# Optimization experiments

Hardware: AMD Instinct MI355X
Metric: run time of the kernel (lower is better)

## Reference

```python
import jax, jax.numpy as jnp
import numpy as np

B, L1, L2, D = 64, 512, 512, 256
NEG_INF = -1e10


def _leaky(x):
    return jax.nn.leaky_relu(x, negative_slope=0.01)


def setup_inputs() -> dict:
    key = jax.random.key(0)
    ks = jax.random.split(key, 12)
    s = 1.0 / np.sqrt(D)
    s2 = 1.0 / np.sqrt(2 * D)
    return {
        "r1": jax.random.normal(ks[0], (B, L1, D), jnp.float32),
        "r2": jax.random.normal(ks[1], (B, L2, D), jnp.float32),
        "mask1": jax.random.randint(ks[2], (B, L1, 1), 0, 2, jnp.int32),
        "mask2": jax.random.randint(ks[3], (B, L2, 1), 0, 2, jnp.int32),
        # mlp params (shared for r1 and r2, as in the torch module)
        "W1": jax.random.uniform(ks[4], (D, D), jnp.float32, -s, s),
        "b1": jnp.zeros((D,), jnp.float32),
        "W2": jax.random.uniform(ks[5], (D, D), jnp.float32, -s, s),
        "b2": jnp.zeros((D,), jnp.float32),
        # compare params
        "Wc1": jax.random.uniform(ks[6], (2 * D, D), jnp.float32, -s2, s2),
        "bc1": jnp.zeros((D,), jnp.float32),
        "Wc2": jax.random.uniform(ks[7], (D, D), jnp.float32, -s, s),
        "bc2": jnp.zeros((D,), jnp.float32),
    }


def _mlp(x, W1, b1, W2, b2):
    return _leaky(_leaky(x @ W1 + b1) @ W2 + b2)


def _compare(x, Wc1, bc1, Wc2, bc2):
    return _leaky(_leaky(x @ Wc1 + bc1) @ Wc2 + bc2)


def reference(r1, r2, mask1, mask2, W1, b1, W2, b2, Wc1, bc1, Wc2, bc2):
    # dropout layers are identity in eval mode
    m1 = mask1.astype(jnp.float32)  # [B,L1,1]
    m2 = mask2.astype(jnp.float32)  # [B,L2,1]

    h1 = _mlp(r1, W1, b1, W2, b2) * m1  # [B,L1,D]
    h2 = _mlp(r2, W1, b1, W2, b2) * m2  # [B,L2,D]

    lens1 = m1.sum(axis=1)  # [B,1]
    lens2 = m2.sum(axis=1)  # [B,1]

    # pairwise validity: matmul of expanded masks is D * outer(m1, m2);
    # only the sign is used downstream.
    pair = m1[:, :, 0][:, :, None] * m2[:, :, 0][:, None, :]  # [B,L1,L2]
    valid = pair > 0
    mask_inf = jnp.where(valid, 0.0, NEG_INF)

    o = jnp.einsum('bld,bmd->blm', h1, h2) + mask_inf  # [B,L1,L2]
    vf = valid.astype(o.dtype)
    o1 = jax.nn.softmax(o, axis=2) * vf
    o2 = jax.nn.softmax(o, axis=1) * vf

    r1_c = jnp.einsum('blm,bmd->bld', o1, h2)  # [B,L1,D]
    r2_c = jnp.einsum('blm,bld->bmd', o2, h1)  # [B,L2,D]

    r1_cmp = _compare(jnp.concatenate([h1, r1_c], axis=-1), Wc1, bc1, Wc2, bc2)
    r2_cmp = _compare(jnp.concatenate([h2, r2_c], axis=-1), Wc1, bc1, Wc2, bc2)

    r1_pool = (r1_cmp * m1).sum(axis=1) / lens1  # [B,D]
    r2_pool = (r2_cmp * m2).sum(axis=1) / lens2  # [B,D]
    return (r1_pool, r2_pool)
```

## Files before the change

### kernel.cpp

```cpp
#include <hip/hip_runtime.h>
#include <math.h>


using frag  = __attribute__((ext_vector_type(8))) short;
using f32x4 = __attribute__((ext_vector_type(4))) float;

constexpr long E = 16777216L;

__device__ __forceinline__ float leaky(float x){ return x > 0.f ? x : 0.01f * x; }

__device__ __forceinline__ unsigned bf16_rne(float f){
    unsigned x = __float_as_uint(f);
    return (x + 0x7fffu + ((x >> 16) & 1u)) >> 16;
}

__device__ __forceinline__ void gload16(const void* g, void* l){
    __builtin_amdgcn_global_load_lds((const __attribute__((address_space(1))) void*)g,
                                     (__attribute__((address_space(3))) void*)l, 16, 0, 0);
}

template<int AMODE, int BMODE, int EPI, int DUALA>
__global__ __launch_bounds__(512, 4)
void gemm_k(const short* __restrict__ pa, const short* __restrict__ pa2,
            const short* __restrict__ pb, const float* __restrict__ bias,
            short* __restrict__ pc,
            const int* __restrict__ mk1, const int* __restrict__ mk2,
            int K, int K1, int lda, int ldb, int ldc,
            long sA, long sB, long sC, long PSA, long PSB, long PSC)
{
    __shared__ __align__(16) short Ah[4096], Al[4096], Bh[4096], Bl[4096];
    const int z = blockIdx.z;
    const int m0 = blockIdx.x * 128, n0 = blockIdx.y * 128;
    const int tid = threadIdx.x, lane = tid & 63, w = tid >> 6;
    const int wr = w >> 2, wc = w & 3;
    const long aoff = (long)z * sA, boff = (long)z * sB, coff = (long)z * sC;

    f32x4 acc[4][2];
#pragma unroll
    for (int i = 0; i < 4; ++i)
#pragma unroll
        for (int j = 0; j < 2; ++j) acc[i][j] = (f32x4){0.f, 0.f, 0.f, 0.f};

    for (int k0 = 0; k0 < K; k0 += 32) {
        if (AMODE == 0) {
            const short* base = pa + aoff; int kk = k0;
            if (DUALA) { if (k0 >= K1) { base = pa2 + aoff; kk = k0 - K1; } }
            const short* s = base + (long)(m0 + w * 16 + (lane & 15)) * lda + kk + (lane >> 4) * 8;
            gload16(s,       &Ah[w * 512]);
            gload16(s + PSA, &Al[w * 512]);
        } else {
            const int gr = m0 + w * 16 + (lane & 15);
            const float* f = (gr < 32768 ? (const float*)pa + (long)gr * lda
                                         : (const float*)pa2 + (long)(gr - 32768) * lda)
                             + k0 + (lane >> 4) * 8;
            float4 u = *(const float4*)f, v4 = *(const float4*)(f + 4);
            float fv[8] = {u.x, u.y, u.z, u.w, v4.x, v4.y, v4.z, v4.w};
            unsigned hu[8], lu[8];
#pragma unroll
            for (int j = 0; j < 8; ++j) {
                hu[j] = bf16_rne(fv[j]);
                lu[j] = bf16_rne(fv[j] - __uint_as_float(hu[j] << 16));
            }
            uint4 hs = {hu[0] | (hu[1] << 16), hu[2] | (hu[3] << 16), hu[4] | (hu[5] << 16), hu[6] | (hu[7] << 16)};
            uint4 ls = {lu[0] | (lu[1] << 16), lu[2] | (lu[3] << 16), lu[4] | (lu[5] << 16), lu[6] | (lu[7] << 16)};
            *(uint4*)&Ah[w * 512 + lane * 8] = hs;
            *(uint4*)&Al[w * 512 + lane * 8] = ls;
        }
        if (BMODE == 0) {
            const short* s = pb + boff + (long)(n0 + w * 16 + (lane & 15)) * ldb + k0 + (lane >> 4) * 8;
            gload16(s,       &Bh[w * 512]);
            gload16(s + PSB, &Bl[w * 512]);
        } else {
            const int kg = tid >> 7, nn = tid & 127;
            const short* s = pb + boff + (long)(k0 + kg * 8) * ldb + n0 + nn;
            unsigned hh[8], ll[8];
#pragma unroll
            for (int i = 0; i < 8; ++i) {
                hh[i] = (unsigned short)s[(long)i * ldb];
                ll[i] = (unsigned short)s[(long)i * ldb + PSB];
            }
            uint4 hw = {hh[0] | (hh[1] << 16), hh[2] | (hh[3] << 16), hh[4] | (hh[5] << 16), hh[6] | (hh[7] << 16)};
            uint4 lw = {ll[0] | (ll[1] << 16), ll[2] | (ll[3] << 16), ll[4] | (ll[5] << 16), ll[6] | (ll[7] << 16)};
            const int d = (nn >> 4) * 512 + (kg * 16 + (nn & 15)) * 8;
            *(uint4*)&Bh[d] = hw;
            *(uint4*)&Bl[d] = lw;
        }
        __syncthreads();

        frag fah[4], fal[4], fbh[2], fbl[2];
#pragma unroll
        for (int mi = 0; mi < 4; ++mi) {
            const int off = (wr * 4 + mi) * 512 + lane * 8;
            fah[mi] = *(const frag*)&Ah[off];
            fal[mi] = *(const frag*)&Al[off];
        }
#pragma unroll
        for (int ni = 0; ni < 2; ++ni) {
            const int off = (wc * 2 + ni) * 512 + lane * 8;
            fbh[ni] = *(const frag*)&Bh[off];
            fbl[ni] = *(const frag*)&Bl[off];
        }
#pragma unroll
        for (int mi = 0; mi < 4; ++mi)
#pragma unroll
            for (int ni = 0; ni < 2; ++ni) {
                acc[mi][ni] = __builtin_amdgcn_mfma_f32_16x16x32_bf16(fah[mi], fbh[ni], acc[mi][ni], 0, 0, 0);
                acc[mi][ni] = __builtin_amdgcn_mfma_f32_16x16x32_bf16(fah[mi], fbl[ni], acc[mi][ni], 0, 0, 0);
                acc[mi][ni] = __builtin_amdgcn_mfma_f32_16x16x32_bf16(fal[mi], fbh[ni], acc[mi][ni], 0, 0, 0);
            }
        __syncthreads();
    }

    float bvv[2];
    if (EPI == 2 || EPI == 3 || EPI == 4) {
#pragma unroll
        for (int ni = 0; ni < 2; ++ni) bvv[ni] = bias[n0 + wc * 32 + ni * 16 + (lane & 15)];
    }
#pragma unroll
    for (int mi = 0; mi < 4; ++mi)
#pragma unroll
        for (int ni = 0; ni < 2; ++ni) {
            const int col = n0 + wc * 32 + ni * 16 + (lane & 15);
#pragma unroll
            for (int r = 0; r < 4; ++r) {
                const int row = m0 + wr * 64 + mi * 16 + (lane >> 4) * 4 + r;
                float v = acc[mi][ni][r];
                if (EPI == 2 || EPI == 3 || EPI == 4) v = leaky(v + bvv[ni]);
                if (EPI == 3) v *= (float)(row < 32768 ? mk1[row] : mk2[row - 32768]);
                const long off = coff + (long)row * ldc + col;
                if (EPI == 0 || EPI == 4) {
                    ((float*)pc)[off] = v;
                } else {
                    unsigned hu = bf16_rne(v);
                    pc[off]       = (short)hu;
                    pc[off + PSC] = (short)bf16_rne(v - __uint_as_float(hu << 16));
                }
            }
        }
}

__global__ __launch_bounds__(256)
void wconv_k(const float* __restrict__ W, short* __restrict__ T, int Kd, long PS)
{
    const int idx = blockIdx.x * 256 + threadIdx.x;
    const int n = idx & 255, k = idx >> 8;
    const float v = W[idx];
    const unsigned hu = bf16_rne(v);
    T[(long)n * Kd + k]      = (short)hu;
    T[(long)n * Kd + k + PS] = (short)bf16_rne(v - __uint_as_float(hu << 16));
}

__global__ __launch_bounds__(256)
void softmax_row_k(const float* __restrict__ S, const int* __restrict__ m1,
                   const int* __restrict__ m2, short* __restrict__ O)
{
    const int tid = threadIdx.x;
    const int wid = tid >> 6, lane = tid & 63;
    const int gr = blockIdx.x * 4 + wid;
    const int b = gr >> 9, l = gr & 511;
    const float* srow = S + (long)gr * 512;
    short* orow = O + (long)gr * 512;
    const int rowvalid = m1[(long)b * 512 + l];
    const int* m2b = m2 + (long)b * 512;
    const int c8 = lane * 8;
    int4 ma = *(const int4*)(m2b + c8);
    int4 mb_ = *(const int4*)(m2b + c8 + 4);
    float4 va = *(const float4*)(srow + c8);
    float4 vb = *(const float4*)(srow + c8 + 4);
    float v[8] = {va.x, va.y, va.z, va.w, vb.x, vb.y, vb.z, vb.w};
    int mk[8] = {ma.x, ma.y, ma.z, ma.w, mb_.x, mb_.y, mb_.z, mb_.w};
    float mx = -3e38f;
#pragma unroll
    for (int j = 0; j < 8; ++j) if (mk[j]) mx = fmaxf(mx, v[j]);
#pragma unroll
    for (int o = 32; o; o >>= 1) mx = fmaxf(mx, __shfl_xor(mx, o));
    if (!rowvalid || mx < -1e30f) {
        uint4 zz = {0u, 0u, 0u, 0u};
        *(uint4*)&orow[c8] = zz;
        *(uint4*)&orow[c8 + E] = zz;
        return;
    }
    float e[8]; float s = 0.f;
#pragma unroll
    for (int j = 0; j < 8; ++j) { e[j] = mk[j] ? __expf(v[j] - mx) : 0.f; s += e[j]; }
#pragma unroll
    for (int o = 32; o; o >>= 1) s += __shfl_xor(s, o);
    const float inv = 1.f / s;
    unsigned short oh[8], ol[8];
#pragma unroll
    for (int j = 0; j < 8; ++j) {
        float p = e[j] * inv;
        unsigned hu = bf16_rne(p);
        oh[j] = (unsigned short)hu;
        ol[j] = (unsigned short)bf16_rne(p - __uint_as_float(hu << 16));
    }
    uint4 hs = {oh[0] | ((unsigned)oh[1] << 16), oh[2] | ((unsigned)oh[3] << 16),
                oh[4] | ((unsigned)oh[5] << 16), oh[6] | ((unsigned)oh[7] << 16)};
    uint4 ls = {ol[0] | ((unsigned)ol[1] << 16), ol[2] | ((unsigned)ol[3] << 16),
                ol[4] | ((unsigned)ol[5] << 16), ol[6] | ((unsigned)ol[7] << 16)};
    *(uint4*)&orow[c8] = hs;
    *(uint4*)&orow[c8 + E] = ls;
}

__global__ __launch_bounds__(1024)
void softmax_col_k(const float* __restrict__ S, const int* __restrict__ m1,
                   const int* __restrict__ m2, short* __restrict__ O)
{
    __shared__ float red[16][64];
    __shared__ int m1s[512];
    __shared__ unsigned tile[64][65];
    const int b = blockIdx.y;
    const int c0 = blockIdx.x * 64;
    const int tid = threadIdx.x;
    const int c = tid & 63, rq = tid >> 6;
    if (tid < 512) m1s[tid] = m1[(long)b * 512 + tid];
    const int ac = m2[(long)b * 512 + c0 + c];
    const float* Sb = S + (long)b * 262144 + c0 + c;
    __syncthreads();

    float v[32];
#pragma unroll
    for (int g = 0; g < 32; ++g) {
        const int r = g * 16 + rq;
        float val = Sb[(long)r * 512];
        v[g] = m1s[r] ? val : -3e38f;
    }
    float mx = -3e38f;
#pragma unroll
    for (int g = 0; g < 32; ++g) mx = fmaxf(mx, v[g]);
    red[rq][c] = mx;
    __syncthreads();
    float M = -3e38f;
#pragma unroll
    for (int i = 0; i < 16; ++i) M = fmaxf(M, red[i][c]);
    __syncthreads();
    float s = 0.f;
#pragma unroll
    for (int g = 0; g < 32; ++g) {
        float e = (v[g] > -1e30f) ? __expf(v[g] - M) : 0.f;
        v[g] = e;
        s += e;
    }
    red[rq][c] = s;
    __syncthreads();
    s = 0.f;
#pragma unroll
    for (int i = 0; i < 16; ++i) s += red[i][c];
    const float inv = (ac && s > 0.f) ? 1.f / s : 0.f;

    const int oc_ = tid >> 4, or_ = tid & 15;
    short* obase = O + (long)b * 262144 + (long)(c0 + oc_) * 512;
    for (int ch = 0; ch < 8; ++ch) {
        __syncthreads();
#pragma unroll
        for (int gg = 0; gg < 4; ++gg) {
            float p = v[ch * 4 + gg] * inv;
            unsigned hu = bf16_rne(p);
            unsigned lu = bf16_rne(p - __uint_as_float(hu << 16));
            tile[c][gg * 16 + rq] = (hu << 16) | lu;
        }
        __syncthreads();
        const unsigned w0 = tile[oc_][or_ * 4 + 0], w1 = tile[oc_][or_ * 4 + 1];
        const unsigned w2 = tile[oc_][or_ * 4 + 2], w3 = tile[oc_][or_ * 4 + 3];
        uint2 ph = { (w0 >> 16) | (w1 & 0xffff0000u), (w2 >> 16) | (w3 & 0xffff0000u) };
        uint2 pl = { (w0 & 0xffffu) | (w1 << 16),     (w2 & 0xffffu) | (w3 << 16) };
        *(uint2*)&obase[ch * 64 + or_ * 4]     = ph;
        *(uint2*)&obase[E + ch * 64 + or_ * 4] = pl;
    }
}

__global__ __launch_bounds__(256)
void pool_part_k(const float* __restrict__ RC, const int* __restrict__ m1,
                 const int* __restrict__ m2, float* __restrict__ part)
{
    const int rs = blockIdx.x, b = blockIdx.y, seg = blockIdx.z;
    const int* mb = (seg ? m2 : m1) + (long)b * 512;
    const float* base = RC + ((long)seg * 32768 + (long)b * 512) * 256;
    const int n = threadIdx.x;
    float acc = 0.f;
    for (int l = rs * 64; l < rs * 64 + 64; ++l)
        if (mb[l]) acc += base[(long)l * 256 + n];
    part[(((long)seg * 64 + b) * 8 + rs) * 256 + n] = acc;
}

__global__ __launch_bounds__(256)
void pool_red_k(const float* __restrict__ part, const int* __restrict__ m1,
                const int* __restrict__ m2, float* __restrict__ out)
{
    __shared__ float cr[256];
    const int g = blockIdx.x;
    const int seg = g >> 6, b = g & 63;
    const int n = threadIdx.x;
    const int* mb = (seg ? m2 : m1) + (long)b * 512;
    float s = 0.f;
#pragma unroll
    for (int i = 0; i < 8; ++i) s += part[((long)g * 8 + i) * 256 + n];
    cr[n] = (float)(mb[n] + mb[n + 256]);
    __syncthreads();
    for (int o = 128; o; o >>= 1) { if (n < o) cr[n] += cr[n + o]; __syncthreads(); }
    out[(long)g * 256 + n] = s / cr[0];
}

extern "C" void kernel_launch(void* const* d_in, const int* in_sizes, int n_in,
                              void* d_out, int out_size, void* d_ws, size_t ws_size,
                              hipStream_t stream)
{
    const float* r1  = (const float*)d_in[0];
    const float* r2  = (const float*)d_in[1];
    const int*   mk1 = (const int*)d_in[2];
    const int*   mk2 = (const int*)d_in[3];
    const float* W1  = (const float*)d_in[4];
    const float* b1  = (const float*)d_in[5];
    const float* W2  = (const float*)d_in[6];
    const float* b2  = (const float*)d_in[7];
    const float* Wc1 = (const float*)d_in[8];
    const float* bc1 = (const float*)d_in[9];
    const float* Wc2 = (const float*)d_in[10];
    const float* bc2 = (const float*)d_in[11];
    float* out = (float*)d_out;

    short* S0s = (short*)d_ws;
    short* S1s = S0s + 2 * E;
    short* S2s = S0s + 4 * E;
    short* S3s = S0s + 6 * E;
    short* Wt1  = S0s;
    short* Wt2  = S0s + 131072;
    short* WtC1 = S1s;
    short* WtC2 = S1s + 262144;
    const long H2 = 8388608;

    wconv_k<<<256, 256, 0, stream>>>(W1, Wt1, 256, 65536);
    wconv_k<<<256, 256, 0, stream>>>(W2, Wt2, 256, 65536);
    gemm_k<1,0,2,0><<<dim3(512,2,1), 512, 0, stream>>>(
        (const short*)r1, (const short*)r2, Wt1, b1, S1s, nullptr, nullptr,
        256, 0, 256, 256, 256, 0, 0, 0, 0, 65536, E);
    gemm_k<0,0,3,0><<<dim3(512,2,1), 512, 0, stream>>>(
        S1s, nullptr, Wt2, b2, S2s, mk1, mk2,
        256, 0, 256, 256, 256, 0, 0, 0, E, 65536, E);
    gemm_k<0,0,0,0><<<dim3(4,4,64), 512, 0, stream>>>(
        S2s, nullptr, S2s + H2, nullptr, S0s, nullptr, nullptr,
        256, 0, 256, 256, 512, 131072, 131072, 262144, E, E, 0);
    softmax_col_k<<<dim3(8,64), 1024, 0, stream>>>((const float*)S0s, mk1, mk2, S1s);
    softmax_row_k<<<8192, 256, 0, stream>>>((const float*)S0s, mk1, mk2, S3s);
    gemm_k<0,1,1,0><<<dim3(4,2,64), 512, 0, stream>>>(
        S3s, nullptr, S2s + H2, nullptr, S0s, nullptr, nullptr,
        512, 0, 512, 256, 256, 262144, 131072, 131072, E, E, E);
    gemm_k<0,1,1,0><<<dim3(4,2,64), 512, 0, stream>>>(
        S1s, nullptr, S2s, nullptr, S0s + H2, nullptr, nullptr,
        512, 0, 512, 256, 256, 262144, 131072, 131072, E, E, E);
    wconv_k<<<512, 256, 0, stream>>>(Wc1, WtC1, 512, 131072);
    wconv_k<<<256, 256, 0, stream>>>(Wc2, WtC2, 256, 65536);
    gemm_k<0,0,2,1><<<dim3(512,2,1), 512, 0, stream>>>(
        S2s, S0s, WtC1, bc1, S3s, nullptr, nullptr,
        512, 256, 256, 512, 256, 0, 0, 0, E, 131072, E);
    gemm_k<0,0,4,0><<<dim3(512,2,1), 512, 0, stream>>>(
        S3s, nullptr, WtC2, bc2, S2s, nullptr, nullptr,
        256, 0, 256, 256, 256, 0, 0, 0, E, 65536, 0);
    pool_part_k<<<dim3(8,64,2), 256, 0, stream>>>((const float*)S2s, mk1, mk2, (float*)S0s);
    pool_red_k<<<128, 256, 0, stream>>>((const float*)S0s, mk1, mk2, out);
}
```

Before: 555.2 us.

## Double-buffer LDS tiles in split-bf16 GEMM to overlap loads with MFMA

Doubles the shared-memory A/B hi/lo tiles and prefetches the next K-slice into the alternate buffer while the current one feeds the MFMAs, dropping one barrier per iteration. The aim is to hide global-to-LDS latency behind the matrix math. LDS use doubles to 64KB per block, which with launch_bounds(512,4) may cut the number of resident blocks per CU. The async global_load_lds writes to the next buffer can overlap with the current reads without extra waits.

```diff
diff --git a/kernel.cpp b/kernel.cpp
--- a/kernel.cpp
+++ b/kernel.cpp
@@ -28,26 +28,20 @@
             int K, int K1, int lda, int ldb, int ldc,
             long sA, long sB, long sC, long PSA, long PSB, long PSC)
 {
-    __shared__ __align__(16) short Ah[4096], Al[4096], Bh[4096], Bl[4096];
+    __shared__ __align__(16) short Ah[2][4096], Al[2][4096], Bh[2][4096], Bl[2][4096];
     const int z = blockIdx.z;
     const int m0 = blockIdx.x * 128, n0 = blockIdx.y * 128;
     const int tid = threadIdx.x, lane = tid & 63, w = tid >> 6;
     const int wr = w >> 2, wc = w & 3;
     const long aoff = (long)z * sA, boff = (long)z * sB, coff = (long)z * sC;
 
-    f32x4 acc[4][2];
-#pragma unroll
-    for (int i = 0; i < 4; ++i)
-#pragma unroll
-        for (int j = 0; j < 2; ++j) acc[i][j] = (f32x4){0.f, 0.f, 0.f, 0.f};
-
-    for (int k0 = 0; k0 < K; k0 += 32) {
+    const auto stage = [&](int buf, int k0) {
         if (AMODE == 0) {
             const short* base = pa + aoff; int kk = k0;
             if (DUALA) { if (k0 >= K1) { base = pa2 + aoff; kk = k0 - K1; } }
             const short* s = base + (long)(m0 + w * 16 + (lane & 15)) * lda + kk + (lane >> 4) * 8;
-            gload16(s,       &Ah[w * 512]);
-            gload16(s + PSA, &Al[w * 512]);
+            gload16(s,       &Ah[buf][w * 512]);
+            gload16(s + PSA, &Al[buf][w * 512]);
         } else {
             const int gr = m0 + w * 16 + (lane & 15);
             const float* f = (gr < 32768 ? (const float*)pa + (long)gr * lda
@@ -63,13 +57,13 @@
             }
             uint4 hs = {hu[0] | (hu[1] << 16), hu[2] | (hu[3] << 16), hu[4] | (hu[5] << 16), hu[6] | (hu[7] << 16)};
             uint4 ls = {lu[0] | (lu[1] << 16), lu[2] | (lu[3] << 16), lu[4] | (lu[5] << 16), lu[6] | (lu[7] << 16)};
-            *(uint4*)&Ah[w * 512 + lane * 8] = hs;
-            *(uint4*)&Al[w * 512 + lane * 8] = ls;
+            *(uint4*)&Ah[buf][w * 512 + lane * 8] = hs;
+            *(uint4*)&Al[buf][w * 512 + lane * 8] = ls;
         }
         if (BMODE == 0) {
             const short* s = pb + boff + (long)(n0 + w * 16 + (lane & 15)) * ldb + k0 + (lane >> 4) * 8;
-            gload16(s,       &Bh[w * 512]);
-            gload16(s + PSB, &Bl[w * 512]);
+            gload16(s,       &Bh[buf][w * 512]);
+            gload16(s + PSB, &Bl[buf][w * 512]);
         } else {
             const int kg = tid >> 7, nn = tid & 127;
             const short* s = pb + boff + (long)(k0 + kg * 8) * ldb + n0 + nn;
@@ -82,23 +76,36 @@
             uint4 hw = {hh[0] | (hh[1] << 16), hh[2] | (hh[3] << 16), hh[4] | (hh[5] << 16), hh[6] | (hh[7] << 16)};
             uint4 lw = {ll[0] | (ll[1] << 16), ll[2] | (ll[3] << 16), ll[4] | (ll[5] << 16), ll[6] | (ll[7] << 16)};
             const int d = (nn >> 4) * 512 + (kg * 16 + (nn & 15)) * 8;
-            *(uint4*)&Bh[d] = hw;
-            *(uint4*)&Bl[d] = lw;
-        }
-        __syncthreads();
+            *(uint4*)&Bh[buf][d] = hw;
+            *(uint4*)&Bl[buf][d] = lw;
+        }
+    };
+
+    f32x4 acc[4][2];
+#pragma unroll
+    for (int i = 0; i < 4; ++i)
+#pragma unroll
+        for (int j = 0; j < 2; ++j) acc[i][j] = (f32x4){0.f, 0.f, 0.f, 0.f};
+
+    stage(0, 0);
+    __syncthreads();
+
+    int cur = 0;
+    for (int k0 = 0; k0 < K; k0 += 32) {
+        if (k0 + 32 < K) stage(cur ^ 1, k0 + 32);
 
         frag fah[4], fal[4], fbh[2], fbl[2];
 #pragma unroll
         for (int mi = 0; mi < 4; ++mi) {
             const int off = (wr * 4 + mi) * 512 + lane * 8;
-            fah[mi] = *(const frag*)&Ah[off];
-            fal[mi] = *(const frag*)&Al[off];
+            fah[mi] = *(const frag*)&Ah[cur][off];
+            fal[mi] = *(const frag*)&Al[cur][off];
         }
 #pragma unroll
         for (int ni = 0; ni < 2; ++ni) {
             const int off = (wc * 2 + ni) * 512 + lane * 8;
-            fbh[ni] = *(const frag*)&Bh[off];
-            fbl[ni] = *(const frag*)&Bl[off];
+            fbh[ni] = *(const frag*)&Bh[cur][off];
+            fbl[ni] = *(const frag*)&Bl[cur][off];
         }
 #pragma unroll
         for (int mi = 0; mi < 4; ++mi)
@@ -109,6 +116,7 @@
                 acc[mi][ni] = __builtin_amdgcn_mfma_f32_16x16x32_bf16(fal[mi], fbh[ni], acc[mi][ni], 0, 0, 0);
             }
         __syncthreads();
+        cur ^= 1;
     }
 
     float bvv[2];
```

Result: faster. 540.9 us (-2.6%).
